# Performance work log

Measured on AMD Instinct MI355X. Metric: run time of the kernel, lower is better.

Reference implementation:

```python
import jax, jax.numpy as jnp
import numpy as np

B, T, C, H = 64, 256, 384, 6
HS = C // H  # 64
EPS = 1e-3  # keras LayerNormalization default epsilon


def layernorm(x, gamma, beta):
    mu = jnp.mean(x, axis=-1, keepdims=True)
    var = jnp.var(x, axis=-1, keepdims=True)
    return (x - mu) * jax.lax.rsqrt(var + EPS) * gamma + beta


def setup_inputs() -> dict:
    key = jax.random.key(0)
    ks = jax.random.split(key, 12)
    s = lambda fan_in: 1.0 / np.sqrt(fan_in)
    return {
        "x": jax.random.normal(ks[0], (B, T, C), dtype=jnp.float32),
        "Wq": jax.random.normal(ks[1], (H, C, HS), dtype=jnp.float32) * s(C),
        "Wk": jax.random.normal(ks[2], (H, C, HS), dtype=jnp.float32) * s(C),
        "Wv": jax.random.normal(ks[3], (H, C, HS), dtype=jnp.float32) * s(C),
        "Wp": jax.random.normal(ks[4], (C, C), dtype=jnp.float32) * s(C),
        "bp": jnp.zeros((C,), dtype=jnp.float32),
        "W1": jax.random.normal(ks[5], (C, 4 * C), dtype=jnp.float32) * s(C),
        "b1": jnp.zeros((4 * C,), dtype=jnp.float32),
        "W2": jax.random.normal(ks[6], (4 * C, C), dtype=jnp.float32) * s(4 * C),
        "b2": jnp.zeros((C,), dtype=jnp.float32),
        "g1": jnp.ones((C,), dtype=jnp.float32),
        "be1": jnp.zeros((C,), dtype=jnp.float32),
        "g2": jnp.ones((C,), dtype=jnp.float32),
        "be2": jnp.zeros((C,), dtype=jnp.float32),
    }


def reference(x, Wq, Wk, Wv, Wp, bp, W1, b1, W2, b2, g1, be1, g2, be2):
    # --- self-attention sub-block (dropout is identity at inference) ---
    h = layernorm(x, g1, be1)                              # [B,T,C]
    q = jnp.einsum('btc,hcd->bhtd', h, Wq)                 # [B,H,T,HS]
    k = jnp.einsum('btc,hcd->bhtd', h, Wk)
    v = jnp.einsum('btc,hcd->bhtd', h, Wv)
    scale = HS ** -0.5
    wei = jnp.einsum('bhtd,bhsd->bhts', q, k) * scale      # [B,H,T,T]
    causal = jnp.tril(jnp.ones((T, T), dtype=bool))
    wei = jnp.where(causal[None, None], wei, -jnp.inf)
    att = jax.nn.softmax(wei, axis=-1)
    o = jnp.einsum('bhts,bhsd->bthd', att, v).reshape(B, T, C)  # concat heads
    sa = o @ Wp + bp
    x = x + sa
    # --- feed-forward sub-block ---
    h2 = layernorm(x, g2, be2)
    ff = jax.nn.relu(h2 @ W1 + b1) @ W2 + b2
    return x + ff
```

## Files before the change

### kernel.cpp

```cpp
#include <hip/hip_runtime.h>
#include <hip/hip_bf16.h>
#include <math.h>

#define Bn 64
#define Tn 256
#define Cn 384
#define Hn 6
#define HSn 64
#define FFn 1536
#define EPSn 1e-3f
#define SECn 6291456

typedef __attribute__((ext_vector_type(4))) float f32x4;
typedef __attribute__((ext_vector_type(2))) float f32x2;
typedef __attribute__((ext_vector_type(8))) short short8;
typedef __attribute__((ext_vector_type(4))) short short4v;
typedef __attribute__((ext_vector_type(2))) short short2v;

__device__ __forceinline__ void async_copy16(void* lds, const void* g) {
    __builtin_amdgcn_global_load_lds(
        (const __attribute__((address_space(1))) void*)g,
        (__attribute__((address_space(3))) void*)lds, 16, 0, 0);
}

__device__ __forceinline__ short f2bf(float v) {
    __hip_bfloat16 h = __float2bfloat16(v);
    return *(short*)&h;
}


__global__ __launch_bounds__(256) void ln_pack_kernel(const float* __restrict__ x,
                                                      const float* __restrict__ g,
                                                      const float* __restrict__ be,
                                                      __hip_bfloat16* __restrict__ outPk) {
    int mt = blockIdx.x;
    int tid = threadIdx.x;
    int lane = tid & 63, wave = tid >> 6;
    __shared__ short rows[16 * 392];
#pragma unroll
    for (int i = 0; i < 4; i++) {
        int r = wave * 4 + i;
        const float* xr = x + ((size_t)mt * 16 + r) * Cn;
        f32x4 a = *(const f32x4*)(xr + lane * 4);
        f32x2 b = *(const f32x2*)(xr + 256 + lane * 2);
        float s = a.x + a.y + a.z + a.w + b.x + b.y;
#pragma unroll
        for (int off = 32; off; off >>= 1) s += __shfl_xor(s, off);
        float mu = s * (1.0f / Cn);
        f32x4 da = a - mu;
        f32x2 db = b - mu;
        float sq = da.x * da.x + da.y * da.y + da.z * da.z + da.w * da.w + db.x * db.x + db.y * db.y;
#pragma unroll
        for (int off = 32; off; off >>= 1) sq += __shfl_xor(sq, off);
        float rs = rsqrtf(sq * (1.0f / Cn) + EPSn);
        f32x4 g4 = *(const f32x4*)(g + lane * 4);
        f32x2 g2 = *(const f32x2*)(g + 256 + lane * 2);
        f32x4 e4 = *(const f32x4*)(be + lane * 4);
        f32x2 e2 = *(const f32x2*)(be + 256 + lane * 2);
        f32x4 y4 = da * rs * g4 + e4;
        f32x2 y2 = db * rs * g2 + e2;
        short4v o4 = {f2bf(y4.x), f2bf(y4.y), f2bf(y4.z), f2bf(y4.w)};
        *(short4v*)(&rows[r * 392 + lane * 4]) = o4;
        short2v o2 = {f2bf(y2.x), f2bf(y2.y)};
        *(short2v*)(&rows[r * 392 + 256 + lane * 2]) = o2;
    }
    __syncthreads();
    int r = lane & 15, q = lane >> 4;
#pragma unroll
    for (int p = 0; p < 3; p++) {
        int f = p * 4 + (tid >> 6);
        short8 v = *(const short8*)(&rows[r * 392 + f * 32 + q * 8]);
        *(short8*)((short*)outPk + ((size_t)mt * 12 + f) * 512 + lane * 8) = v;
    }
}

__global__ __launch_bounds__(256) void pack_b_kernel(const float* __restrict__ W,
                                                     __hip_bfloat16* __restrict__ out,
                                                     int K, int N) {
    int id = blockIdx.x * 256 + threadIdx.x;
    if (id >= K * N) return;
    int tile = id >> 9, lane = (id >> 3) & 63, j = id & 7;
    int ntiles = N >> 4;
    int k = (tile / ntiles) * 32 + ((lane >> 4) << 3) + j;
    int n = (tile % ntiles) * 16 + (lane & 15);
    out[id] = __float2bfloat16(W[(size_t)k * N + n]);
}

__global__ __launch_bounds__(256) void pack_qkv_kernel(const float* __restrict__ Wq,
                                                       const float* __restrict__ Wk,
                                                       const float* __restrict__ Wv,
                                                       __hip_bfloat16* __restrict__ out) {
    int id = blockIdx.x * 256 + threadIdx.x;
    if (id >= Cn * 1152) return;
    int tile = id >> 9, lane = (id >> 3) & 63, j = id & 7;
    int k = (tile / 72) * 32 + ((lane >> 4) << 3) + j;
    int n = (tile % 72) * 16 + (lane & 15);
    int sec = n / Cn, rem = n % Cn;
    int hh = rem >> 6, d = rem & 63;
    const float* W = (sec == 0) ? Wq : ((sec == 1) ? Wk : Wv);
    out[id] = __float2bfloat16(W[((size_t)hh * Cn + k) * HSn + d]);
}

template <int KK, int NN, int EPI>
__global__ __launch_bounds__(256) void gemm_mfma(const __hip_bfloat16* __restrict__ Apk,
                                                 const __hip_bfloat16* __restrict__ Bp,
                                                 const float* __restrict__ bias,
                                                 const float* __restrict__ resid,
                                                 float* __restrict__ outF,
                                                 __hip_bfloat16* __restrict__ outB) {
    constexpr int GX = NN / 64;
    constexpr int K32 = KK / 32;
    constexpr int NC = K32 / 4;
    constexpr int NT16 = NN / 16;
    __shared__ __align__(16) short ldsB[2 * 8192];

    int l = blockIdx.x;
    int xcd = l & 7, i = l >> 3;
    int rowblk = xcd * 16 + i / GX;
    int colblk = i - (i / GX) * GX;

    int lane = threadIdx.x & 63, wave = threadIdx.x >> 6;
    int lrow = lane & 15, lquad = lane >> 4;
    int m0 = rowblk * 128;
    int n0 = colblk * 64;
    int mt0 = (m0 >> 4) + wave * 2;

    f32x4 acc[2][4];
#pragma unroll
    for (int st = 0; st < 2; st++)
#pragma unroll
        for (int nt = 0; nt < 4; nt++) acc[st][nt] = (f32x4){0.f, 0.f, 0.f, 0.f};

    const short* a0p = (const short*)Apk + ((size_t)mt0 * K32) * 512 + lane * 8;
    const short* a1p = a0p + (size_t)K32 * 512;
    const short* bsrc = (const short*)Bp + ((size_t)wave * NT16 + (n0 >> 4)) * 512 + lane * 8;
    short* bdst0 = ldsB + wave * 2048;

#pragma unroll
    for (int nt = 0; nt < 4; nt++) async_copy16(bdst0 + nt * 512, bsrc + nt * 512);
    short8 aR[2][2][4];
#pragma unroll
    for (int kf = 0; kf < 4; kf++) {
        aR[0][0][kf] = *(const short8*)(a0p + kf * 512);
        aR[0][1][kf] = *(const short8*)(a1p + kf * 512);
    }

#pragma unroll
    for (int c = 0; c < NC; c++) {
        __syncthreads();
        if (c + 1 < NC) {
            const short* bs = bsrc + (size_t)(c + 1) * 4 * NT16 * 512;
            short* bd = ldsB + ((c + 1) & 1) * 8192 + wave * 2048;
#pragma unroll
            for (int nt = 0; nt < 4; nt++) async_copy16(bd + nt * 512, bs + nt * 512);
#pragma unroll
            for (int kf = 0; kf < 4; kf++) {
                aR[(c + 1) & 1][0][kf] = *(const short8*)(a0p + ((c + 1) * 4 + kf) * 512);
                aR[(c + 1) & 1][1][kf] = *(const short8*)(a1p + ((c + 1) * 4 + kf) * 512);
            }
        }
        const short* bl = ldsB + (c & 1) * 8192 + lane * 8;
#pragma unroll
        for (int kf = 0; kf < 4; kf++) {
#pragma unroll
            for (int nt = 0; nt < 4; nt++) {
                short8 bf = *(const short8*)(bl + (kf * 4 + nt) * 512);
                acc[0][nt] = __builtin_amdgcn_mfma_f32_16x16x32_bf16(aR[c & 1][0][kf], bf,
                                                                     acc[0][nt], 0, 0, 0);
                acc[1][nt] = __builtin_amdgcn_mfma_f32_16x16x32_bf16(aR[c & 1][1][kf], bf,
                                                                     acc[1][nt], 0, 0, 0);
            }
        }
    }
    __syncthreads();

    if (EPI == 1) {
        float* twf = (float*)((char*)ldsB + wave * 4864);
        float bnv[4];
#pragma unroll
        for (int nt = 0; nt < 4; nt++) bnv[nt] = bias[n0 + nt * 16 + lrow];
#pragma unroll
        for (int st = 0; st < 2; st++) {
            int mbase = m0 + (2 * wave + st) * 16;
#pragma unroll
            for (int nt = 0; nt < 4; nt++)
#pragma unroll
                for (int r = 0; r < 4; r++)
                    twf[(lquad * 4 + r) * 76 + nt * 16 + lrow] = acc[st][nt][r] + bnv[nt];
            int row = lane >> 2, seg = lane & 3;
            int m = mbase + row;
            const float* rrow = resid + (size_t)m * NN + n0 + seg * 16;
            float* orow = outF + (size_t)m * NN + n0 + seg * 16;
#pragma unroll
            for (int c = 0; c < 4; c++) {
                f32x4 vv = *(const f32x4*)(&twf[row * 76 + seg * 16 + c * 4]);
                f32x4 rv = *(const f32x4*)(rrow + c * 4);
                *(f32x4*)(orow + c * 4) = vv + rv;
            }
            __builtin_amdgcn_s_waitcnt(0);
        }
    } else {
        short* tws = (short*)((char*)ldsB + wave * 4864);
        float bnv[4];
        if (EPI == 2) {
#pragma unroll
            for (int nt = 0; nt < 4; nt++) bnv[nt] = bias[n0 + nt * 16 + lrow];
        }
#pragma unroll
        for (int st = 0; st < 2; st++)
#pragma unroll
            for (int nt = 0; nt < 4; nt++)
#pragma unroll
                for (int r = 0; r < 4; r++) {
                    float v = acc[st][nt][r];
                    if (EPI == 2) v = fmaxf(v + bnv[nt], 0.0f);
                    tws[(st * 16 + lquad * 4 + r) * 72 + nt * 16 + lrow] = f2bf(v);
                }
        if (EPI == 2) {
#pragma unroll
            for (int st2 = 0; st2 < 2; st2++) {
                int mt = (m0 >> 4) + wave * 2 + st2;
#pragma unroll
                for (int kcl = 0; kcl < 2; kcl++) {
                    int kc = (n0 >> 5) + kcl;
                    short8 v = *(const short8*)(
                        &tws[(st2 * 16 + (lane & 15)) * 72 + kcl * 32 + (lane >> 4) * 8]);
                    *(short8*)((short*)outB + ((size_t)mt * (NN / 32) + kc) * 512 + lane * 8) = v;
                }
            }
        } else {
            int sec = n0 / 384;
            int rem0 = n0 - sec * 384;
            int hh = rem0 >> 6;
            int b = m0 >> 8;
            int t_base = (m0 & 255) + wave * 32;
            int bh2 = b * Hn + hh;
            if (sec < 2) {
                short* outp = (short*)outB + (size_t)sec * SECn + (size_t)bh2 * 16384 +
                              (size_t)(t_base >> 4) * 1024 + lane * 8;
#pragma unroll
                for (int st2 = 0; st2 < 2; st2++)
#pragma unroll
                    for (int kc = 0; kc < 2; kc++) {
                        short8 v8 = *(const short8*)(
                            &tws[(st2 * 16 + (lane & 15)) * 72 + kc * 32 + (lane >> 4) * 8]);
                        *(short8*)(outp + (st2 * 2 + kc) * 512) = v8;
                    }
            } else {
                short* vout = (short*)outB + (size_t)2 * SECn + (size_t)bh2 * 16384 +
                              (size_t)((t_base >> 5) * 4) * 512;
#pragma unroll
                for (int dt = 0; dt < 4; dt++) {
                    short8 v8;
#pragma unroll
                    for (int j = 0; j < 8; j++) {
                        int t_loc = ((lane >> 4) << 3) + j;
                        v8[j] = tws[t_loc * 72 + dt * 16 + (lane & 15)];
                    }
                    *(short8*)(vout + dt * 512 + lane * 8) = v8;
                }
            }
        }
    }
}

__global__ __launch_bounds__(256) void attn_mfma_kernel(const __hip_bfloat16* __restrict__ qp,
                                                        const __hip_bfloat16* __restrict__ kp,
                                                        const __hip_bfloat16* __restrict__ vp,
                                                        __hip_bfloat16* __restrict__ o) {
    __shared__ short Kl[16 * 1024];
    __shared__ short Pl[4 * 2048];
    int blk = blockIdx.x;
    int bh = blk % (Bn * Hn);
    int jg = blk / (Bn * Hn);
    int b = bh / Hn, hh = bh - b * Hn;
    int tid = threadIdx.x;
    int lane = tid & 63, wave = tid >> 6;
    int c16 = lane & 15, quad = lane >> 4;
    int qt = (wave << 2) + ((wave & 1) ? (3 - jg) : jg);

    const short* ks = (const short*)kp + (size_t)bh * 16384;
#pragma unroll
    for (int i = 0; i < 8; i++) {
        int tile = wave * 8 + i;
        async_copy16(&Kl[tile * 512], ks + tile * 512 + lane * 8);
    }

    const short* qs = (const short*)qp + (size_t)bh * 16384 + (size_t)qt * 1024 + lane * 8;
    const short* vs = (const short*)vp + (size_t)bh * 16384 + lane * 8;
    short* Pw = Pl + wave * 2048;

    short8 aq0 = *(const short8*)(qs);
    short8 aq1 = *(const short8*)(qs + 512);

    int st_max = qt;
    int kb_count = (qt + 2) >> 1;
    int covered = kb_count * 2;
    int qrow0 = qt * 16;

    __syncthreads();

    f32x4 accS[16];
#pragma unroll
    for (int st = 0; st < 16; st++) accS[st] = (f32x4){0.f, 0.f, 0.f, 0.f};
#pragma unroll
    for (int st = 0; st < 16; st++) {
        if (st <= st_max) {
            short8 bk0 = *(const short8*)(&Kl[st * 1024 + lane * 8]);
            short8 bk1 = *(const short8*)(&Kl[st * 1024 + 512 + lane * 8]);
            accS[st] = __builtin_amdgcn_mfma_f32_16x16x32_bf16(aq0, bk0, accS[st], 0, 0, 0);
            accS[st] = __builtin_amdgcn_mfma_f32_16x16x32_bf16(aq1, bk1, accS[st], 0, 0, 0);
        }
    }

    float mx[4];
#pragma unroll
    for (int r = 0; r < 4; r++) {
        int row = qrow0 + quad * 4 + r;
        float m = -INFINITY;
#pragma unroll
        for (int st = 0; st < 16; st++) {
            if (st <= st_max) {
                int col = st * 16 + c16;
                float a = (col <= row) ? accS[st][r] * 0.125f : -INFINITY;
                accS[st][r] = a;
                m = fmaxf(m, a);
            }
        }
#pragma unroll
        for (int off = 8; off; off >>= 1) m = fmaxf(m, __shfl_xor(m, off));
        mx[r] = m;
    }

    float sum[4] = {0.f, 0.f, 0.f, 0.f};
    f32x4 accO[4];
#pragma unroll
    for (int nt = 0; nt < 4; nt++) accO[nt] = (f32x4){0.f, 0.f, 0.f, 0.f};
#pragma unroll
    for (int half = 0; half < 2; half++) {
        int st_lo = half * 8;
        if (st_lo < covered) {
#pragma unroll
            for (int st2 = 0; st2 < 8; st2++) {
                int st = st_lo + st2;
                if (st < covered) {
#pragma unroll
                    for (int r = 0; r < 4; r++) {
                        float e = 0.0f;
                        if (st <= st_max) {
                            e = __expf(accS[st][r] - mx[r]);
                            sum[r] += e;
                        }
                        int cl = st2 * 16 + c16;
                        Pw[(cl >> 5) * 512 + (((cl >> 3) & 3) * 16 + quad * 4 + r) * 8 +
                           (cl & 7)] = f2bf(e);
                    }
                }
            }
#pragma unroll
            for (int k2 = 0; k2 < 4; k2++) {
                int kbi = half * 4 + k2;
                if (kbi < kb_count) {
                    short8 ap = *(const short8*)(Pw + k2 * 512 + lane * 8);
#pragma unroll
                    for (int nt = 0; nt < 4; nt++) {
                        short8 bv = *(const short8*)(vs + (kbi * 4 + nt) * 512);
                        accO[nt] = __builtin_amdgcn_mfma_f32_16x16x32_bf16(ap, bv, accO[nt],
                                                                           0, 0, 0);
                    }
                }
            }
        }
    }

    float inv[4];
#pragma unroll
    for (int r = 0; r < 4; r++) {
        float s = sum[r];
#pragma unroll
        for (int off = 8; off; off >>= 1) s += __shfl_xor(s, off);
        inv[r] = 1.0f / s;
    }

#pragma unroll
    for (int nt = 0; nt < 4; nt++)
#pragma unroll
        for (int r = 0; r < 4; r++)
            Pw[(quad * 4 + r) * 72 + nt * 16 + c16] = f2bf(accO[nt][r] * inv[r]);
    int mt = (b << 4) + qt;
#pragma unroll
    for (int kcl = 0; kcl < 2; kcl++) {
        short8 v = *(const short8*)(&Pw[(lane & 15) * 72 + kcl * 32 + (lane >> 4) * 8]);
        *(short8*)((short*)o + ((size_t)mt * 12 + hh * 2 + kcl) * 512 + lane * 8) = v;
    }
}

extern "C" void kernel_launch(void* const* d_in, const int* in_sizes, int n_in,
                              void* d_out, int out_size, void* d_ws, size_t ws_size,
                              hipStream_t stream) {
    const float* x  = (const float*)d_in[0];
    const float* Wq = (const float*)d_in[1];
    const float* Wk = (const float*)d_in[2];
    const float* Wv = (const float*)d_in[3];
    const float* Wp = (const float*)d_in[4];
    const float* bp = (const float*)d_in[5];
    const float* W1 = (const float*)d_in[6];
    const float* b1 = (const float*)d_in[7];
    const float* W2 = (const float*)d_in[8];
    const float* b2 = (const float*)d_in[9];
    const float* g1 = (const float*)d_in[10];
    const float* be1 = (const float*)d_in[11];
    const float* g2 = (const float*)d_in[12];
    const float* be2 = (const float*)d_in[13];

    const size_t M = (size_t)Bn * Tn;
    __hip_bfloat16* ws  = (__hip_bfloat16*)d_ws;
    __hip_bfloat16* h   = ws;
    __hip_bfloat16* big = h + M * Cn;
    __hip_bfloat16* o   = big + M * FFn;
    __hip_bfloat16* pQKV = o + M * Cn;
    __hip_bfloat16* pWp  = pQKV + Cn * 1152;
    __hip_bfloat16* pW1  = pWp + Cn * Cn;
    __hip_bfloat16* pW2  = pW1 + Cn * FFn;

    float* x2 = (float*)d_out;

    pack_qkv_kernel<<<(Cn * 1152 + 255) / 256, 256, 0, stream>>>(Wq, Wk, Wv, pQKV);
    pack_b_kernel<<<(Cn * Cn + 255) / 256, 256, 0, stream>>>(Wp, pWp, Cn, Cn);
    pack_b_kernel<<<(Cn * FFn + 255) / 256, 256, 0, stream>>>(W1, pW1, Cn, FFn);
    pack_b_kernel<<<(FFn * Cn + 255) / 256, 256, 0, stream>>>(W2, pW2, FFn, Cn);

    ln_pack_kernel<<<M / 16, 256, 0, stream>>>(x, g1, be1, h);
    gemm_mfma<Cn, 1152, 0><<<2304, 256, 0, stream>>>(h, pQKV, nullptr, nullptr, nullptr, big);
    attn_mfma_kernel<<<Bn * Hn * 4, 256, 0, stream>>>(big, big + SECn, big + 2 * SECn, o);
    gemm_mfma<Cn, Cn, 1><<<768, 256, 0, stream>>>(o, pWp, bp, x, x2, nullptr);
    ln_pack_kernel<<<M / 16, 256, 0, stream>>>(x2, g2, be2, h);
    gemm_mfma<Cn, FFn, 2><<<3072, 256, 0, stream>>>(h, pW1, b1, nullptr, nullptr, big);
    gemm_mfma<FFn, Cn, 1><<<768, 256, 0, stream>>>(big, pW2, b2, x2, x2, nullptr);
}
```

Baseline: 243.4 us.

## Add K=384 GEMM variant staging full B tile in LDS with register-prefetched A

Adds a specialized GEMM kernel for K=384 that loads the whole 384x64 B panel into LDS once with a single barrier, and streams A fragments straight from global memory into registers, double-buffered in groups of three k-steps. It also sets launch bounds allowing three blocks per CU. The QKV, output projection and FFN-up GEMMs now use it, which removes the per-chunk LDS double-buffering and barrier overhead of the generic kernel. The generic kernel keeps only the W2 GEMM, and its QKV epilogue branch is removed. Risks include register pressure from the held A fragments and lower occupancy from the larger LDS footprint.

```diff
diff --git a/kernel.cpp b/kernel.cpp
--- a/kernel.cpp
+++ b/kernel.cpp
@@ -101,6 +101,170 @@
     out[id] = __float2bfloat16(W[((size_t)hh * Cn + k) * HSn + d]);
 }
 
+template <int NN, int EPI>
+__global__ __launch_bounds__(256, 3) void gemm_persist(const __hip_bfloat16* __restrict__ Apk,
+                                                       const __hip_bfloat16* __restrict__ Bp,
+                                                       const float* __restrict__ bias,
+                                                       const float* __restrict__ resid,
+                                                       float* __restrict__ outF,
+                                                       __hip_bfloat16* __restrict__ outB) {
+    constexpr int GX = NN / 64;
+    constexpr int K32 = 12;
+    constexpr int NT16 = NN / 16;
+    __shared__ __align__(16) short ldsB[48 * 512];
+
+    int l = blockIdx.x;
+    int xcd = l & 7, i = l >> 3;
+    int rowblk = xcd * 16 + i / GX;
+    int colblk = i - (i / GX) * GX;
+
+    int lane = threadIdx.x & 63, wave = threadIdx.x >> 6;
+    int lrow = lane & 15, lquad = lane >> 4;
+    int m0 = rowblk * 128;
+    int n0 = colblk * 64;
+    int mt0 = (m0 >> 4) + wave * 2;
+
+    {
+        const short* bbase = (const short*)Bp + (size_t)(n0 >> 4) * 512 + lane * 8;
+#pragma unroll
+        for (int t = 0; t < 12; t++) {
+            int idx = wave * 12 + t;
+            int kf = idx >> 2, ntl = idx & 3;
+            async_copy16(&ldsB[idx * 512], bbase + ((size_t)kf * NT16 + ntl) * 512);
+        }
+    }
+
+    f32x4 acc[2][4];
+#pragma unroll
+    for (int st = 0; st < 2; st++)
+#pragma unroll
+        for (int nt = 0; nt < 4; nt++) acc[st][nt] = (f32x4){0.f, 0.f, 0.f, 0.f};
+
+    const short* a0p = (const short*)Apk + ((size_t)mt0 * K32) * 512 + lane * 8;
+    const short* a1p = a0p + (size_t)K32 * 512;
+
+    short8 af[2][2][3];
+#pragma unroll
+    for (int kf = 0; kf < 3; kf++) {
+        af[0][0][kf] = *(const short8*)(a0p + kf * 512);
+        af[0][1][kf] = *(const short8*)(a1p + kf * 512);
+    }
+    __syncthreads();
+
+#pragma unroll
+    for (int q = 0; q < 4; q++) {
+        if (q < 3) {
+#pragma unroll
+            for (int kf = 0; kf < 3; kf++) {
+                af[(q + 1) & 1][0][kf] = *(const short8*)(a0p + ((q + 1) * 3 + kf) * 512);
+                af[(q + 1) & 1][1][kf] = *(const short8*)(a1p + ((q + 1) * 3 + kf) * 512);
+            }
+        }
+#pragma unroll
+        for (int kf = 0; kf < 3; kf++) {
+            int kfa = q * 3 + kf;
+#pragma unroll
+            for (int nt = 0; nt < 4; nt++) {
+                short8 bf = *(const short8*)(&ldsB[(kfa * 4 + nt) * 512 + lane * 8]);
+                acc[0][nt] = __builtin_amdgcn_mfma_f32_16x16x32_bf16(af[q & 1][0][kf], bf,
+                                                                     acc[0][nt], 0, 0, 0);
+                acc[1][nt] = __builtin_amdgcn_mfma_f32_16x16x32_bf16(af[q & 1][1][kf], bf,
+                                                                     acc[1][nt], 0, 0, 0);
+            }
+        }
+    }
+    __syncthreads();
+
+    if (EPI == 1) {
+        float* twf = (float*)((char*)ldsB + wave * 4864);
+        float bnv[4];
+#pragma unroll
+        for (int nt = 0; nt < 4; nt++) bnv[nt] = bias[n0 + nt * 16 + lrow];
+#pragma unroll
+        for (int st = 0; st < 2; st++) {
+            int mbase = m0 + (2 * wave + st) * 16;
+#pragma unroll
+            for (int nt = 0; nt < 4; nt++)
+#pragma unroll
+                for (int r = 0; r < 4; r++)
+                    twf[(lquad * 4 + r) * 76 + nt * 16 + lrow] = acc[st][nt][r] + bnv[nt];
+            int row = lane >> 2, seg = lane & 3;
+            int m = mbase + row;
+            const float* rrow = resid + (size_t)m * NN + n0 + seg * 16;
+            float* orow = outF + (size_t)m * NN + n0 + seg * 16;
+#pragma unroll
+            for (int c = 0; c < 4; c++) {
+                f32x4 vv = *(const f32x4*)(&twf[row * 76 + seg * 16 + c * 4]);
+                f32x4 rv = *(const f32x4*)(rrow + c * 4);
+                *(f32x4*)(orow + c * 4) = vv + rv;
+            }
+            __builtin_amdgcn_s_waitcnt(0);
+        }
+    } else {
+        short* tws = (short*)((char*)ldsB + wave * 4864);
+        float bnv[4];
+        if (EPI == 2) {
+#pragma unroll
+            for (int nt = 0; nt < 4; nt++) bnv[nt] = bias[n0 + nt * 16 + lrow];
+        }
+#pragma unroll
+        for (int st = 0; st < 2; st++)
+#pragma unroll
+            for (int nt = 0; nt < 4; nt++)
+#pragma unroll
+                for (int r = 0; r < 4; r++) {
+                    float v = acc[st][nt][r];
+                    if (EPI == 2) v = fmaxf(v + bnv[nt], 0.0f);
+                    tws[(st * 16 + lquad * 4 + r) * 72 + nt * 16 + lrow] = f2bf(v);
+                }
+        if (EPI == 2) {
+#pragma unroll
+            for (int st2 = 0; st2 < 2; st2++) {
+                int mt = (m0 >> 4) + wave * 2 + st2;
+#pragma unroll
+                for (int kcl = 0; kcl < 2; kcl++) {
+                    int kc = (n0 >> 5) + kcl;
+                    short8 v = *(const short8*)(
+                        &tws[(st2 * 16 + (lane & 15)) * 72 + kcl * 32 + (lane >> 4) * 8]);
+                    *(short8*)((short*)outB + ((size_t)mt * (NN / 32) + kc) * 512 + lane * 8) = v;
+                }
+            }
+        } else {
+            int sec = n0 / 384;
+            int rem0 = n0 - sec * 384;
+            int hh = rem0 >> 6;
+            int b = m0 >> 8;
+            int t_base = (m0 & 255) + wave * 32;
+            int bh2 = b * Hn + hh;
+            if (sec < 2) {
+                short* outp = (short*)outB + (size_t)sec * SECn + (size_t)bh2 * 16384 +
+                              (size_t)(t_base >> 4) * 1024 + lane * 8;
+#pragma unroll
+                for (int st2 = 0; st2 < 2; st2++)
+#pragma unroll
+                    for (int kc = 0; kc < 2; kc++) {
+                        short8 v8 = *(const short8*)(
+                            &tws[(st2 * 16 + (lane & 15)) * 72 + kc * 32 + (lane >> 4) * 8]);
+                        *(short8*)(outp + (st2 * 2 + kc) * 512) = v8;
+                    }
+            } else {
+                short* vout = (short*)outB + (size_t)2 * SECn + (size_t)bh2 * 16384 +
+                              (size_t)((t_base >> 5) * 4) * 512;
+#pragma unroll
+                for (int dt = 0; dt < 4; dt++) {
+                    short8 v8;
+#pragma unroll
+                    for (int j = 0; j < 8; j++) {
+                        int t_loc = ((lane >> 4) << 3) + j;
+                        v8[j] = tws[t_loc * 72 + dt * 16 + (lane & 15)];
+                    }
+                    *(short8*)(vout + dt * 512 + lane * 8) = v8;
+                }
+            }
+        }
+    }
+}
+
 template <int KK, int NN, int EPI>
 __global__ __launch_bounds__(256) void gemm_mfma(const __hip_bfloat16* __restrict__ Apk,
                                                  const __hip_bfloat16* __restrict__ Bp,
@@ -226,38 +390,6 @@
                     short8 v = *(const short8*)(
                         &tws[(st2 * 16 + (lane & 15)) * 72 + kcl * 32 + (lane >> 4) * 8]);
                     *(short8*)((short*)outB + ((size_t)mt * (NN / 32) + kc) * 512 + lane * 8) = v;
-                }
-            }
-        } else {
-            int sec = n0 / 384;
-            int rem0 = n0 - sec * 384;
-            int hh = rem0 >> 6;
-            int b = m0 >> 8;
-            int t_base = (m0 & 255) + wave * 32;
-            int bh2 = b * Hn + hh;
-            if (sec < 2) {
-                short* outp = (short*)outB + (size_t)sec * SECn + (size_t)bh2 * 16384 +
-                              (size_t)(t_base >> 4) * 1024 + lane * 8;
-#pragma unroll
-                for (int st2 = 0; st2 < 2; st2++)
-#pragma unroll
-                    for (int kc = 0; kc < 2; kc++) {
-                        short8 v8 = *(const short8*)(
-                            &tws[(st2 * 16 + (lane & 15)) * 72 + kc * 32 + (lane >> 4) * 8]);
-                        *(short8*)(outp + (st2 * 2 + kc) * 512) = v8;
-                    }
-            } else {
-                short* vout = (short*)outB + (size_t)2 * SECn + (size_t)bh2 * 16384 +
-                              (size_t)((t_base >> 5) * 4) * 512;
-#pragma unroll
-                for (int dt = 0; dt < 4; dt++) {
-                    short8 v8;
-#pragma unroll
-                    for (int j = 0; j < 8; j++) {
-                        int t_loc = ((lane >> 4) << 3) + j;
-                        v8[j] = tws[t_loc * 72 + dt * 16 + (lane & 15)];
-                    }
-                    *(short8*)(vout + dt * 512 + lane * 8) = v8;
                 }
             }
         }
@@ -431,10 +563,10 @@
     pack_b_kernel<<<(FFn * Cn + 255) / 256, 256, 0, stream>>>(W2, pW2, FFn, Cn);
 
     ln_pack_kernel<<<M / 16, 256, 0, stream>>>(x, g1, be1, h);
-    gemm_mfma<Cn, 1152, 0><<<2304, 256, 0, stream>>>(h, pQKV, nullptr, nullptr, nullptr, big);
+    gemm_persist<1152, 0><<<2304, 256, 0, stream>>>(h, pQKV, nullptr, nullptr, nullptr, big);
     attn_mfma_kernel<<<Bn * Hn * 4, 256, 0, stream>>>(big, big + SECn, big + 2 * SECn, o);
-    gemm_mfma<Cn, Cn, 1><<<768, 256, 0, stream>>>(o, pWp, bp, x, x2, nullptr);
+    gemm_persist<Cn, 1><<<768, 256, 0, stream>>>(o, pWp, bp, x, x2, nullptr);
     ln_pack_kernel<<<M / 16, 256, 0, stream>>>(x2, g2, be2, h);
-    gemm_mfma<Cn, FFn, 2><<<3072, 256, 0, stream>>>(h, pW1, b1, nullptr, nullptr, big);
+    gemm_persist<FFn, 2><<<3072, 256, 0, stream>>>(h, pW1, b1, nullptr, nullptr, big);
     gemm_mfma<FFn, Cn, 1><<<768, 256, 0, stream>>>(big, pW2, b2, x2, x2, nullptr);
 }
```

After: 247.1 us. Within noise of the previous version (+1.5%).
